# Kernel tuning notes

Measured on AMD Instinct MI355X. Metric: run time of the kernel, lower is better.

## Reference

```python
import jax, jax.numpy as jnp
import numpy as np

B, C, H, W = 128, 2048, 14, 14
K = 112          # num_concepts
NUM_CLASSES = 200


def setup_inputs() -> dict:
    key = jax.random.key(0)
    ks = jax.random.split(key, 8)
    x = jax.random.normal(ks[0], (B, C, H, W), dtype=jnp.float32)
    concepts = jax.random.normal(ks[1], (K, C), dtype=jnp.float32)
    modulation = jax.random.normal(ks[2], (1, C), dtype=jnp.float32)
    background = jax.random.normal(ks[3], (1, C), dtype=jnp.float32)
    # concept_fc: Linear(C, 1)
    w_cfc = jax.random.normal(ks[4], (1, C), dtype=jnp.float32) / np.sqrt(C)
    b_cfc = jnp.zeros((1,), dtype=jnp.float32)
    # label_fc: Linear(C*K, num_classes)
    w_lfc = jax.random.normal(ks[5], (NUM_CLASSES, C * K), dtype=jnp.float32) / np.sqrt(C * K)
    b_lfc = jnp.zeros((NUM_CLASSES,), dtype=jnp.float32)
    return {"x": x, "concepts": concepts, "modulation": modulation,
            "background": background, "w_cfc": w_cfc, "b_cfc": b_cfc,
            "w_lfc": w_lfc, "b_lfc": b_lfc}


def reference(x, concepts, modulation, background, w_cfc, b_cfc, w_lfc, b_lfc):
    b, c, h, w = x.shape
    n = h * w
    x_flat = x.reshape(b, c, n).transpose(0, 2, 1)          # [b, n, c]
    cpts_wbg = jnp.concatenate([concepts, background], 0)   # [k+1, c]

    # cdist p=2 via ||a||^2 + ||x||^2 - 2 a.x
    a_sq = jnp.sum(cpts_wbg * cpts_wbg, -1)                 # [k+1]
    x_sq = jnp.sum(x_flat * x_flat, -1)                     # [b, n]
    dots = jnp.einsum('kc,bnc->bkn', cpts_wbg, x_flat)      # [b, k+1, n]
    d2 = a_sq[None, :, None] + x_sq[:, None, :] - 2.0 * dots
    dists = jnp.sqrt(jnp.maximum(d2, 0.0))                  # [b, k+1, n]

    attn = jax.nn.softmax(-dists, axis=1)                   # softmax over concepts
    cpt_score_maps = attn.reshape(b, -1, h, w)              # [b, k+1, h, w]

    cpt_reprs = jnp.einsum('bkn,bnc->bkc', attn[:, :-1, :], x_flat)  # [b, k, c]
    cpt_logits = jax.nn.sigmoid(
        jnp.einsum('bkc,oc->bko', cpt_reprs, w_cfc) + b_cfc).squeeze(-1)  # [b, k]

    g = cpt_logits[..., None]                               # [b, k, 1]
    cpts_mixed = g * concepts[None] + (1.0 - g) * modulation[None]  # [b, k, c]
    label_logits = cpts_mixed.reshape(b, -1) @ w_lfc.T + b_lfc      # [b, classes]

    return cpt_score_maps, cpt_logits, label_logits
```

## Files before the change

### kernel.cpp

```cpp
#include <hip/hip_runtime.h>
#include <hip/hip_bf16.h>
#include <math.h>

#define B 128
#define C 2048
#define N 196
#define K 112
#define KB 113
#define MROWS 128
#define XWROW 113
#define NCLS 200
#define CKC (C * K)
#define MAIN_BLKS 128
#define PQ_BLKS 700
#define XSTEP 25088
#define IMGB (C * N * 4)

#define OUT1_OFF 2834944
#define OUT2_OFF 2849280

typedef __attribute__((ext_vector_type(8))) short bf16x8;
typedef __attribute__((ext_vector_type(4))) float f32x4;

__device__ inline unsigned cvtpk(float a, float b) {
    union { __hip_bfloat162 h; unsigned u; } c;
    c.h.x = __float2bfloat16(a);
    c.h.y = __float2bfloat16(b);
    return c.u;
}
__device__ inline const float* row_src(int row, const float* concepts,
                                       const float* background, const float* wcfc) {
    if (row < K) return concepts + (size_t)row * C;
    if (row == K) return background;
    if (row == XWROW) return wcfc;
    return nullptr;
}
__device__ __forceinline__ void gl16(const void* g, void* l) {
    __builtin_amdgcn_global_load_lds(
        (const __attribute__((address_space(1))) unsigned*)g,
        (__attribute__((address_space(3))) unsigned*)l, 16, 0, 0);
}
__device__ __forceinline__ void gl4(const void* g, void* l) {
    __builtin_amdgcn_global_load_lds(
        (const __attribute__((address_space(1))) unsigned*)g,
        (__attribute__((address_space(3))) unsigned*)l, 4, 0, 0);
}

__global__ __launch_bounds__(256)
void asq_kernel(const float* __restrict__ concepts, const float* __restrict__ background,
                const float* __restrict__ wcfc, float* __restrict__ asq) {
    const int row = blockIdx.x;
    const int tid = threadIdx.x;
    const float* src = row_src(row, concepts, background, wcfc);
    float local = 0.f;
    if (src) for (int i = tid; i < C; i += 256) { float v = src[i]; local += v * v; }
    for (int off = 32; off; off >>= 1) local += __shfl_down(local, off);
    __shared__ float red[4];
    if ((tid & 63) == 0) red[tid >> 6] = local;
    __syncthreads();
    if (tid == 0) asq[row] = red[0] + red[1] + red[2] + red[3];
}

__global__ __launch_bounds__(64)
void pack_kernel(const float* __restrict__ concepts, const float* __restrict__ background,
                 const float* __restrict__ wcfc, unsigned short* __restrict__ Afrag) {
    const int f = blockIdx.x;
    const int kwg = blockIdx.y;
    const int l = threadIdx.x;
    const int row = 16 * f + (l & 15);
    const int kb = 32 * kwg + 8 * (l >> 4);
    const float* src = row_src(row, concepts, background, wcfc);
    unsigned o[4] = {0u, 0u, 0u, 0u};
    if (src) {
        const float4 f0 = *reinterpret_cast<const float4*>(src + kb);
        const float4 f1 = *reinterpret_cast<const float4*>(src + kb + 4);
        o[0] = cvtpk(f0.x, f0.y); o[1] = cvtpk(f0.z, f0.w);
        o[2] = cvtpk(f1.x, f1.y); o[3] = cvtpk(f1.z, f1.w);
    }
    *reinterpret_cast<uint4*>(Afrag + (((size_t)kwg * 8 + f) * 64 + l) * 8) =
        make_uint4(o[0], o[1], o[2], o[3]);
}

__global__ __launch_bounds__(512)
void fused_kernel(const float* __restrict__ x,
                  const unsigned short* __restrict__ Afrag,
                  const float* __restrict__ asq_g,
                  float* __restrict__ out0,
                  float* __restrict__ lpart,
                  const float* __restrict__ wlfc,
                  const float* __restrict__ concepts,
                  const float* __restrict__ modulation,
                  float* __restrict__ Rm, float* __restrict__ Qs) {
    __shared__ __align__(16) char smem[61952];
    const int tid = threadIdx.x;
    const int lane = tid & 63;
    const int w = tid >> 6;
    const int blkid = blockIdx.x;

    if (blkid < MAIN_BLKS) {
        const int b = blkid;
        float* Xf = (float*)smem;
        char* Ab0 = smem + 25600;
        unsigned short* XT = (unsigned short*)(smem + 41984);
        float* xsqL = (float*)(smem + 58624);
        float* pmw = (float*)smem;
        float* xwL = (float*)(smem + 8192);

        const int lo = lane & 15, hi = lane >> 4;
        const char* xim = (const char*)x + (size_t)b * IMGB;
        const char* Ag = (const char*)Afrag;

        const bool act = tid < 416;
        const int h = (act && tid >= 208) ? 1 : 0;
        const int cc = act ? (tid - 208 * h) : 0;

        f32x4 acc[13];
#pragma unroll
        for (int ct = 0; ct < 13; ++ct) acc[ct] = (f32x4){0.f, 0.f, 0.f, 0.f};
        float xs = 0.f;

#define ISSUE_X(JJ) do {                                                        \
        const char* sx_ = xim + (size_t)(JJ) * XSTEP;                           \
        gl16(sx_ + (3 * w + 0) * 1024 + lane * 16, smem + (3 * w + 0) * 1024);  \
        gl16(sx_ + (3 * w + 1) * 1024 + lane * 16, smem + (3 * w + 1) * 1024);  \
        gl16(sx_ + (3 * w + 2) * 1024 + lane * 16, smem + (3 * w + 2) * 1024);  \
        if (w < 2) gl4(sx_ + 24576 + w * 256 + lane * 4,                        \
                       smem + 24576 + w * 256);                                 \
    } while (0)

#define ISSUE_A(JJ) do {                                                        \
        gl16(Ag + (size_t)(JJ) * 8192 + w * 1024 + lane * 16,                   \
             Ab0 + ((JJ) & 1) * 8192 + w * 1024);                               \
    } while (0)

#define VM0() do {                                                              \
        asm volatile("s_waitcnt vmcnt(0)" ::: "memory");                        \
        __builtin_amdgcn_sched_barrier(0);                                      \
    } while (0)

#define LBAR() do {                                                             \
        asm volatile("s_waitcnt lgkmcnt(0)" ::: "memory");                      \
        __builtin_amdgcn_s_barrier();                                           \
        __builtin_amdgcn_sched_barrier(0);                                      \
    } while (0)

#define CONVERT() do {                                                          \
        if (act) {                                                              \
            const float* xp_ = Xf + (16 * h) * 196 + cc;                        \
            float v_[16];                                                       \
            _Pragma("unroll")                                                   \
            for (int q_ = 0; q_ < 16; ++q_) v_[q_] = xp_[q_ * 196];             \
            _Pragma("unroll")                                                   \
            for (int q_ = 0; q_ < 16; ++q_) xs += v_[q_] * v_[q_];              \
            unsigned u_[8];                                                     \
            _Pragma("unroll")                                                   \
            for (int p_ = 0; p_ < 8; ++p_)                                      \
                u_[p_] = cvtpk(v_[2 * p_], v_[2 * p_ + 1]);                     \
            unsigned short* xt_ = XT + cc * 40 + h * 16;                        \
            *reinterpret_cast<uint4*>(xt_) = make_uint4(u_[0], u_[1], u_[2], u_[3]); \
            *reinterpret_cast<uint4*>(xt_ + 8) = make_uint4(u_[4], u_[5], u_[6], u_[7]); \
        }                                                                       \
    } while (0)

#define MFMA_STEP(JJ) do {                                                      \
        const char* Ab_ = Ab0 + ((JJ) & 1) * 8192;                              \
        const bf16x8 afr_ = *reinterpret_cast<const bf16x8*>(                   \
            Ab_ + ((w * 64 + lane) << 4));                                      \
        _Pragma("unroll")                                                       \
        for (int ct_ = 0; ct_ < 13; ++ct_) {                                    \
            const bf16x8 bfr_ = *reinterpret_cast<const bf16x8*>(               \
                (const char*)XT + (ct_ * 16 + lo) * 80 + hi * 16);              \
            acc[ct_] = __builtin_amdgcn_mfma_f32_16x16x32_bf16(                 \
                afr_, bfr_, acc[ct_], 0, 0, 0);                                 \
        }                                                                       \
    } while (0)

        ISSUE_X(0); ISSUE_A(0);
#pragma unroll 1
        for (int j = 0; j < 63; ++j) {
            VM0(); LBAR();
            CONVERT();
            LBAR();
            ISSUE_X(j + 1);
            MFMA_STEP(j);
            ISSUE_A(j + 1);
        }
        VM0(); LBAR(); CONVERT(); LBAR(); MFMA_STEP(63);

        __syncthreads();
        if (act) xsqL[h * 208 + cc] = xs;
        if (w == 7 && hi == 0) {
#pragma unroll
            for (int ct = 0; ct < 13; ++ct) xwL[ct * 16 + lo] = acc[ct][1];
        }
        __syncthreads();

        float xq[13];
#pragma unroll
        for (int ct = 0; ct < 13; ++ct) {
            const int c = ct * 16 + lo;
            xq[ct] = xsqL[c] + xsqL[208 + c];
        }
        float aq[4];
#pragma unroll
        for (int rr = 0; rr < 4; ++rr) aq[rr] = asq_g[16 * w + 4 * hi + rr];
        const bool v4 = (w < 7);

        float mct[13];
#pragma unroll
        for (int ct = 0; ct < 13; ++ct) {
#pragma unroll
            for (int rr = 0; rr < 4; ++rr) {
                const float d2 = aq[rr] + xq[ct] - 2.f * acc[ct][rr];
                acc[ct][rr] = -sqrtf(fmaxf(d2, 0.f));
            }
            float mv = -3.4e38f;
            if (v4) mv = fmaxf(fmaxf(acc[ct][0], acc[ct][1]),
                               fmaxf(acc[ct][2], acc[ct][3]));
            else if (hi == 0) mv = acc[ct][0];
            mv = fmaxf(mv, __shfl_xor(mv, 16));
            mv = fmaxf(mv, __shfl_xor(mv, 32));
            mct[ct] = mv;
        }
        if (hi == 0) {
#pragma unroll
            for (int ct = 0; ct < 13; ++ct) pmw[w * 208 + ct * 16 + lo] = mct[ct];
        }
        __syncthreads();
        float Mct[13];
#pragma unroll
        for (int ct = 0; ct < 13; ++ct) {
            float mm = -3.4e38f;
#pragma unroll
            for (int ww = 0; ww < 8; ++ww)
                mm = fmaxf(mm, pmw[ww * 208 + ct * 16 + lo]);
            Mct[ct] = mm;
        }
        __syncthreads();
        float sct[13];
#pragma unroll
        for (int ct = 0; ct < 13; ++ct) {
            float ss = 0.f;
#pragma unroll
            for (int rr = 0; rr < 4; ++rr) {
                const bool valid = v4 || (hi == 0 && rr == 0);
                const float e = valid ? __expf(acc[ct][rr] - Mct[ct]) : 0.f;
                acc[ct][rr] = e;
                ss += e;
            }
            ss += __shfl_xor(ss, 16);
            ss += __shfl_xor(ss, 32);
            sct[ct] = ss;
        }
        if (hi == 0) {
#pragma unroll
            for (int ct = 0; ct < 13; ++ct) pmw[w * 208 + ct * 16 + lo] = sct[ct];
        }
        __syncthreads();
        float inv[13];
#pragma unroll
        for (int ct = 0; ct < 13; ++ct) {
            float SS = 0.f;
#pragma unroll
            for (int ww = 0; ww < 8; ++ww) SS += pmw[ww * 208 + ct * 16 + lo];
            inv[ct] = 1.f / SS;
        }

        float* o0 = out0 + (size_t)b * KB * N;
#pragma unroll
        for (int ct = 0; ct < 13; ++ct) {
            const int c = ct * 16 + lo;
            const bool cv = c < N;
#pragma unroll
            for (int rr = 0; rr < 4; ++rr) {
                const int r = 16 * w + 4 * hi + rr;
                const bool valid = v4 || (hi == 0 && rr == 0);
                if (valid && cv) o0[(size_t)r * N + c] = acc[ct][rr] * inv[ct];
            }
        }
        if (v4) {
#pragma unroll
            for (int rr = 0; rr < 4; ++rr) {
                float pv = 0.f;
#pragma unroll
                for (int ct = 0; ct < 13; ++ct) {
                    const int c = ct * 16 + lo;
                    const float term = acc[ct][rr] * inv[ct] * xwL[c];
                    pv += (c < N) ? term : 0.f;
                }
                pv += __shfl_xor(pv, 1);
                pv += __shfl_xor(pv, 2);
                pv += __shfl_xor(pv, 4);
                pv += __shfl_xor(pv, 8);
                if (lo == 0) lpart[(size_t)b * K + 16 * w + 4 * hi + rr] = pv;
            }
        }
    } else {
        const int wb = (blkid - MAIN_BLKS) * 32 + w * 4;
#pragma unroll
        for (int q = 0; q < 4; ++q) {
            const int wid = wb + q;
            const int o = wid / K;
            const int k = wid % K;
            const float4* wp = reinterpret_cast<const float4*>(wlfc + (size_t)o * CKC + (size_t)k * C);
            const float4* cp = reinterpret_cast<const float4*>(concepts + (size_t)k * C);
            const float4* mp = reinterpret_cast<const float4*>(modulation);
            float s1 = 0.f, s2 = 0.f;
#pragma unroll
            for (int it = 0; it < 8; ++it) {
                const int idx = it * 64 + lane;
                const float4 w4 = wp[idx];
                const float4 c4 = cp[idx];
                const float4 m4 = mp[idx];
                s1 += w4.x * c4.x + w4.y * c4.y + w4.z * c4.z + w4.w * c4.w;
                s2 += w4.x * m4.x + w4.y * m4.y + w4.z * m4.z + w4.w * m4.w;
            }
            for (int off = 32; off; off >>= 1) {
                s1 += __shfl_down(s1, off);
                s2 += __shfl_down(s2, off);
            }
            if (lane == 0) { Rm[wid] = s1 - s2; Qs[wid] = s2; }
        }
    }
}

__global__ __launch_bounds__(256)
void final_kernel(const float* __restrict__ lpart, const float* __restrict__ bcfc,
                  const float* __restrict__ Rm, const float* __restrict__ Qs,
                  const float* __restrict__ blfc,
                  float* __restrict__ out1, float* __restrict__ out2) {
    const int b = blockIdx.x;
    const int tid = threadIdx.x;
    __shared__ float g_s[K];
    if (tid < K) {
        const float v = lpart[(size_t)b * K + tid] + bcfc[0];
        const float g = 1.f / (1.f + __expf(-v));
        out1[b * K + tid] = g;
        g_s[tid] = g;
    }
    __syncthreads();
    if (tid < NCLS) {
        float acc = blfc[tid];
        const float* rp = Rm + (size_t)tid * K;
        const float* qp = Qs + (size_t)tid * K;
        for (int k = 0; k < K; ++k) acc = fmaf(g_s[k], rp[k], acc) + qp[k];
        out2[b * NCLS + tid] = acc;
    }
}

extern "C" void kernel_launch(void* const* d_in, const int* in_sizes, int n_in,
                              void* d_out, int out_size, void* d_ws, size_t ws_size,
                              hipStream_t stream) {
    const float* x          = (const float*)d_in[0];
    const float* concepts   = (const float*)d_in[1];
    const float* modulation = (const float*)d_in[2];
    const float* background = (const float*)d_in[3];
    const float* wcfc       = (const float*)d_in[4];
    const float* bcfc       = (const float*)d_in[5];
    const float* wlfc       = (const float*)d_in[6];
    const float* blfc       = (const float*)d_in[7];

    float* out  = (float*)d_out;
    float* out0 = out;
    float* out1 = out + OUT1_OFF;
    float* out2 = out + OUT2_OFF;

    float* ws    = (float*)d_ws;
    float* asq   = ws;
    float* lpart = asq + MROWS;
    float* Rm    = lpart + (size_t)B * K;
    float* Qs    = Rm + NCLS * K;
    unsigned short* Afrag = (unsigned short*)(Qs + NCLS * K);

    asq_kernel<<<MROWS, 256, 0, stream>>>(concepts, background, wcfc, asq);
    pack_kernel<<<dim3(8, 64), 64, 0, stream>>>(concepts, background, wcfc, Afrag);
    fused_kernel<<<MAIN_BLKS + PQ_BLKS, 512, 0, stream>>>(
        x, Afrag, asq, out0, lpart, wlfc, concepts, modulation, Rm, Qs);
    final_kernel<<<B, 256, 0, stream>>>(lpart, bcfc, Rm, Qs, blfc, out1, out2);
}
```

Measured before the change: 121.3 us.

## Split channel reduction across four blocks per image with atomic accumulation

The main GEMM phase now splits the 2048-channel reduction into four chunks, so each image is handled by four blocks instead of one and grid parallelism grows from 128 to 512 main blocks. Partial dot products, x-squared sums and the background-weight products are accumulated with float atomics into the output buffer and workspace, which are zeroed by memsets beforehand. The distance, softmax and concept-logit epilogue moves to a separate softmax kernel that rereads the accumulated dots. This adds two memsets, one extra launch, many global atomics and an extra read-modify-write pass over the score map, and float atomics make the summation order nondeterministic.

```diff
diff --git a/kernel.cpp b/kernel.cpp
--- a/kernel.cpp
+++ b/kernel.cpp
@@ -11,7 +11,9 @@
 #define XWROW 113
 #define NCLS 200
 #define CKC (C * K)
-#define MAIN_BLKS 128
+#define NSPL 4
+#define ITERS 16
+#define MAIN_BLKS 512
 #define PQ_BLKS 700
 #define XSTEP 25088
 #define IMGB (C * N * 4)
@@ -84,35 +86,32 @@
 __global__ __launch_bounds__(512)
 void fused_kernel(const float* __restrict__ x,
                   const unsigned short* __restrict__ Afrag,
-                  const float* __restrict__ asq_g,
                   float* __restrict__ out0,
-                  float* __restrict__ lpart,
+                  float* __restrict__ xsq_ws, float* __restrict__ xw_ws,
                   const float* __restrict__ wlfc,
                   const float* __restrict__ concepts,
                   const float* __restrict__ modulation,
                   float* __restrict__ Rm, float* __restrict__ Qs) {
-    __shared__ __align__(16) char smem[61952];
+    __shared__ __align__(16) char smem[58624];
     const int tid = threadIdx.x;
     const int lane = tid & 63;
     const int w = tid >> 6;
     const int blkid = blockIdx.x;
 
     if (blkid < MAIN_BLKS) {
-        const int b = blkid;
+        const int b = blkid >> 2;
+        const int h = blkid & 3;
         float* Xf = (float*)smem;
         char* Ab0 = smem + 25600;
         unsigned short* XT = (unsigned short*)(smem + 41984);
-        float* xsqL = (float*)(smem + 58624);
-        float* pmw = (float*)smem;
-        float* xwL = (float*)(smem + 8192);
 
         const int lo = lane & 15, hi = lane >> 4;
         const char* xim = (const char*)x + (size_t)b * IMGB;
         const char* Ag = (const char*)Afrag;
 
         const bool act = tid < 416;
-        const int h = (act && tid >= 208) ? 1 : 0;
-        const int cc = act ? (tid - 208 * h) : 0;
+        const int h2 = (act && tid >= 208) ? 1 : 0;
+        const int cc = act ? (tid - 208 * h2) : 0;
 
         f32x4 acc[13];
 #pragma unroll
@@ -146,7 +145,7 @@
 
 #define CONVERT() do {                                                          \
         if (act) {                                                              \
-            const float* xp_ = Xf + (16 * h) * 196 + cc;                        \
+            const float* xp_ = Xf + (16 * h2) * 196 + cc;                       \
             float v_[16];                                                       \
             _Pragma("unroll")                                                   \
             for (int q_ = 0; q_ < 16; ++q_) v_[q_] = xp_[q_ * 196];             \
@@ -156,7 +155,7 @@
             _Pragma("unroll")                                                   \
             for (int p_ = 0; p_ < 8; ++p_)                                      \
                 u_[p_] = cvtpk(v_[2 * p_], v_[2 * p_ + 1]);                     \
-            unsigned short* xt_ = XT + cc * 40 + h * 16;                        \
+            unsigned short* xt_ = XT + cc * 40 + h2 * 16;                       \
             *reinterpret_cast<uint4*>(xt_) = make_uint4(u_[0], u_[1], u_[2], u_[3]); \
             *reinterpret_cast<uint4*>(xt_ + 8) = make_uint4(u_[4], u_[5], u_[6], u_[7]); \
         }                                                                       \
@@ -175,9 +174,11 @@
         }                                                                       \
     } while (0)
 
-        ISSUE_X(0); ISSUE_A(0);
+        const int j0 = h * ITERS;
+        ISSUE_X(j0); ISSUE_A(j0);
 #pragma unroll 1
-        for (int j = 0; j < 63; ++j) {
+        for (int jj = 0; jj < ITERS - 1; ++jj) {
+            const int j = j0 + jj;
             VM0(); LBAR();
             CONVERT();
             LBAR();
@@ -185,114 +186,23 @@
             MFMA_STEP(j);
             ISSUE_A(j + 1);
         }
-        VM0(); LBAR(); CONVERT(); LBAR(); MFMA_STEP(63);
-
-        __syncthreads();
-        if (act) xsqL[h * 208 + cc] = xs;
-        if (w == 7 && hi == 0) {
-#pragma unroll
-            for (int ct = 0; ct < 13; ++ct) xwL[ct * 16 + lo] = acc[ct][1];
-        }
-        __syncthreads();
-
-        float xq[13];
+        VM0(); LBAR(); CONVERT(); LBAR(); MFMA_STEP(j0 + ITERS - 1);
+
+        if (act) atomicAdd(&xsq_ws[(size_t)b * 208 + cc], xs);
+        const bool v4 = (w < 7);
+        float* od = out0 + (size_t)b * KB * N;
 #pragma unroll
         for (int ct = 0; ct < 13; ++ct) {
             const int c = ct * 16 + lo;
-            xq[ct] = xsqL[c] + xsqL[208 + c];
-        }
-        float aq[4];
-#pragma unroll
-        for (int rr = 0; rr < 4; ++rr) aq[rr] = asq_g[16 * w + 4 * hi + rr];
-        const bool v4 = (w < 7);
-
-        float mct[13];
-#pragma unroll
-        for (int ct = 0; ct < 13; ++ct) {
-#pragma unroll
-            for (int rr = 0; rr < 4; ++rr) {
-                const float d2 = aq[rr] + xq[ct] - 2.f * acc[ct][rr];
-                acc[ct][rr] = -sqrtf(fmaxf(d2, 0.f));
-            }
-            float mv = -3.4e38f;
-            if (v4) mv = fmaxf(fmaxf(acc[ct][0], acc[ct][1]),
-                               fmaxf(acc[ct][2], acc[ct][3]));
-            else if (hi == 0) mv = acc[ct][0];
-            mv = fmaxf(mv, __shfl_xor(mv, 16));
-            mv = fmaxf(mv, __shfl_xor(mv, 32));
-            mct[ct] = mv;
-        }
-        if (hi == 0) {
-#pragma unroll
-            for (int ct = 0; ct < 13; ++ct) pmw[w * 208 + ct * 16 + lo] = mct[ct];
-        }
-        __syncthreads();
-        float Mct[13];
-#pragma unroll
-        for (int ct = 0; ct < 13; ++ct) {
-            float mm = -3.4e38f;
-#pragma unroll
-            for (int ww = 0; ww < 8; ++ww)
-                mm = fmaxf(mm, pmw[ww * 208 + ct * 16 + lo]);
-            Mct[ct] = mm;
-        }
-        __syncthreads();
-        float sct[13];
-#pragma unroll
-        for (int ct = 0; ct < 13; ++ct) {
-            float ss = 0.f;
-#pragma unroll
-            for (int rr = 0; rr < 4; ++rr) {
-                const bool valid = v4 || (hi == 0 && rr == 0);
-                const float e = valid ? __expf(acc[ct][rr] - Mct[ct]) : 0.f;
-                acc[ct][rr] = e;
-                ss += e;
-            }
-            ss += __shfl_xor(ss, 16);
-            ss += __shfl_xor(ss, 32);
-            sct[ct] = ss;
-        }
-        if (hi == 0) {
-#pragma unroll
-            for (int ct = 0; ct < 13; ++ct) pmw[w * 208 + ct * 16 + lo] = sct[ct];
-        }
-        __syncthreads();
-        float inv[13];
-#pragma unroll
-        for (int ct = 0; ct < 13; ++ct) {
-            float SS = 0.f;
-#pragma unroll
-            for (int ww = 0; ww < 8; ++ww) SS += pmw[ww * 208 + ct * 16 + lo];
-            inv[ct] = 1.f / SS;
-        }
-
-        float* o0 = out0 + (size_t)b * KB * N;
-#pragma unroll
-        for (int ct = 0; ct < 13; ++ct) {
-            const int c = ct * 16 + lo;
-            const bool cv = c < N;
-#pragma unroll
-            for (int rr = 0; rr < 4; ++rr) {
-                const int r = 16 * w + 4 * hi + rr;
-                const bool valid = v4 || (hi == 0 && rr == 0);
-                if (valid && cv) o0[(size_t)r * N + c] = acc[ct][rr] * inv[ct];
-            }
-        }
-        if (v4) {
-#pragma unroll
-            for (int rr = 0; rr < 4; ++rr) {
-                float pv = 0.f;
-#pragma unroll
-                for (int ct = 0; ct < 13; ++ct) {
-                    const int c = ct * 16 + lo;
-                    const float term = acc[ct][rr] * inv[ct] * xwL[c];
-                    pv += (c < N) ? term : 0.f;
+            if (c < N) {
+#pragma unroll
+                for (int rr = 0; rr < 4; ++rr) {
+                    const int r = 16 * w + 4 * hi + rr;
+                    if (v4 || (hi == 0 && rr == 0))
+                        atomicAdd(&od[(size_t)r * N + c], acc[ct][rr]);
                 }
-                pv += __shfl_xor(pv, 1);
-                pv += __shfl_xor(pv, 2);
-                pv += __shfl_xor(pv, 4);
-                pv += __shfl_xor(pv, 8);
-                if (lo == 0) lpart[(size_t)b * K + 16 * w + 4 * hi + rr] = pv;
+                if (w == 7 && hi == 0)
+                    atomicAdd(&xw_ws[(size_t)b * 208 + c], acc[ct][1]);
             }
         }
     } else {
@@ -324,6 +234,137 @@
     }
 }
 
+__global__ __launch_bounds__(512)
+void softmax_kernel(float* __restrict__ out0,
+                    const float* __restrict__ xsq_ws, const float* __restrict__ xw_ws,
+                    const float* __restrict__ asq_g,
+                    float* __restrict__ lpart) {
+    __shared__ float pmw[8 * 208];
+    __shared__ float xsqL[208];
+    __shared__ float xwL[208];
+    const int b = blockIdx.x;
+    const int tid = threadIdx.x;
+    const int lane = tid & 63;
+    const int w = tid >> 6;
+    const int lo = lane & 15, hi = lane >> 4;
+
+    if (tid < 208) {
+        xsqL[tid] = xsq_ws[(size_t)b * 208 + tid];
+        xwL[tid] = xw_ws[(size_t)b * 208 + tid];
+    }
+    __syncthreads();
+
+    const bool v4 = (w < 7);
+    float* od = out0 + (size_t)b * KB * N;
+
+    f32x4 acc[13];
+    float aq[4];
+#pragma unroll
+    for (int rr = 0; rr < 4; ++rr) aq[rr] = asq_g[16 * w + 4 * hi + rr];
+
+#pragma unroll
+    for (int ct = 0; ct < 13; ++ct) {
+        const int c = ct * 16 + lo;
+        const bool cv = c < N;
+#pragma unroll
+        for (int rr = 0; rr < 4; ++rr) {
+            const int r = 16 * w + 4 * hi + rr;
+            const bool valid = v4 || (hi == 0 && rr == 0);
+            acc[ct][rr] = (valid && cv) ? od[(size_t)r * N + c] : 0.f;
+        }
+    }
+
+    float mct[13];
+#pragma unroll
+    for (int ct = 0; ct < 13; ++ct) {
+        const int c = ct * 16 + lo;
+#pragma unroll
+        for (int rr = 0; rr < 4; ++rr) {
+            const float d2 = aq[rr] + xsqL[c] - 2.f * acc[ct][rr];
+            acc[ct][rr] = -sqrtf(fmaxf(d2, 0.f));
+        }
+        float mv = -3.4e38f;
+        if (v4) mv = fmaxf(fmaxf(acc[ct][0], acc[ct][1]),
+                           fmaxf(acc[ct][2], acc[ct][3]));
+        else if (hi == 0) mv = acc[ct][0];
+        mv = fmaxf(mv, __shfl_xor(mv, 16));
+        mv = fmaxf(mv, __shfl_xor(mv, 32));
+        mct[ct] = mv;
+    }
+    if (hi == 0) {
+#pragma unroll
+        for (int ct = 0; ct < 13; ++ct) pmw[w * 208 + ct * 16 + lo] = mct[ct];
+    }
+    __syncthreads();
+    float Mct[13];
+#pragma unroll
+    for (int ct = 0; ct < 13; ++ct) {
+        float mm = -3.4e38f;
+#pragma unroll
+        for (int ww = 0; ww < 8; ++ww)
+            mm = fmaxf(mm, pmw[ww * 208 + ct * 16 + lo]);
+        Mct[ct] = mm;
+    }
+    __syncthreads();
+    float sct[13];
+#pragma unroll
+    for (int ct = 0; ct < 13; ++ct) {
+        float ss = 0.f;
+#pragma unroll
+        for (int rr = 0; rr < 4; ++rr) {
+            const bool valid = v4 || (hi == 0 && rr == 0);
+            const float e = valid ? __expf(acc[ct][rr] - Mct[ct]) : 0.f;
+            acc[ct][rr] = e;
+            ss += e;
+        }
+        ss += __shfl_xor(ss, 16);
+        ss += __shfl_xor(ss, 32);
+        sct[ct] = ss;
+    }
+    if (hi == 0) {
+#pragma unroll
+        for (int ct = 0; ct < 13; ++ct) pmw[w * 208 + ct * 16 + lo] = sct[ct];
+    }
+    __syncthreads();
+    float inv[13];
+#pragma unroll
+    for (int ct = 0; ct < 13; ++ct) {
+        float SS = 0.f;
+#pragma unroll
+        for (int ww = 0; ww < 8; ++ww) SS += pmw[ww * 208 + ct * 16 + lo];
+        inv[ct] = 1.f / SS;
+    }
+
+#pragma unroll
+    for (int ct = 0; ct < 13; ++ct) {
+        const int c = ct * 16 + lo;
+        const bool cv = c < N;
+#pragma unroll
+        for (int rr = 0; rr < 4; ++rr) {
+            const int r = 16 * w + 4 * hi + rr;
+            const bool valid = v4 || (hi == 0 && rr == 0);
+            if (valid && cv) od[(size_t)r * N + c] = acc[ct][rr] * inv[ct];
+        }
+    }
+    if (v4) {
+#pragma unroll
+        for (int rr = 0; rr < 4; ++rr) {
+            float pv = 0.f;
+#pragma unroll
+            for (int ct = 0; ct < 13; ++ct) {
+                const int c = ct * 16 + lo;
+                const float term = acc[ct][rr] * inv[ct] * xwL[c];
+                pv += (c < N) ? term : 0.f;
+            }
+            pv += __shfl_xor(pv, 1);
+            pv += __shfl_xor(pv, 2);
+            pv += __shfl_xor(pv, 4);
+            pv += __shfl_xor(pv, 8);
+            if (lo == 0) lpart[(size_t)b * K + 16 * w + 4 * hi + rr] = pv;
+        }
+    }
+}
+
 __global__ __launch_bounds__(256)
 void final_kernel(const float* __restrict__ lpart, const float* __restrict__ bcfc,
                   const float* __restrict__ Rm, const float* __restrict__ Qs,
@@ -365,16 +406,22 @@
     float* out1 = out + OUT1_OFF;
     float* out2 = out + OUT2_OFF;
 
-    float* ws    = (float*)d_ws;
-    float* asq   = ws;
-    float* lpart = asq + MROWS;
-    float* Rm    = lpart + (size_t)B * K;
-    float* Qs    = Rm + NCLS * K;
-    unsigned short* Afrag = (unsigned short*)(Qs + NCLS * K);
+    float* ws     = (float*)d_ws;
+    float* asq    = ws;
+    float* lpart  = asq + MROWS;
+    float* Rm     = lpart + (size_t)B * K;
+    float* Qs     = Rm + NCLS * K;
+    float* xsq_ws = Qs + NCLS * K;
+    float* xw_ws  = xsq_ws + (size_t)B * 208;
+    unsigned short* Afrag = (unsigned short*)(xw_ws + (size_t)B * 208);
+
+    hipMemsetAsync(out0, 0, (size_t)OUT1_OFF * sizeof(float), stream);
+    hipMemsetAsync(xsq_ws, 0, (size_t)2 * B * 208 * sizeof(float), stream);
 
     asq_kernel<<<MROWS, 256, 0, stream>>>(concepts, background, wcfc, asq);
     pack_kernel<<<dim3(8, 64), 64, 0, stream>>>(concepts, background, wcfc, Afrag);
     fused_kernel<<<MAIN_BLKS + PQ_BLKS, 512, 0, stream>>>(
-        x, Afrag, asq, out0, lpart, wlfc, concepts, modulation, Rm, Qs);
+        x, Afrag, out0, xsq_ws, xw_ws, wlfc, concepts, modulation, Rm, Qs);
+    softmax_kernel<<<B, 512, 0, stream>>>(out0, xsq_ws, xw_ws, asq, lpart);
     final_kernel<<<B, 256, 0, stream>>>(lpart, bcfc, Rm, Qs, blfc, out1, out2);
 }
```

Result: slower. 199.5 us (+64.5%).

## Deepen load pipeline and retile MFMA work as 2x2 row/column wave grid

Applied to the files above, without the earlier changes.

The main loop now triple-buffers the fp32 x tiles and quad-buffers the A fragments, issuing loads two steps ahead. It also double-buffers the transposed bf16 tile so the conversion of step j overlaps the MFMA of step j-1, with one barrier per iteration instead of two. Waves are regrouped into a 4x2 grid where each wave computes two row tiles by up to seven column tiles, reusing B fragments across two A fragments. Shared memory grows to about 140KB, which limits occupancy, and the softmax reductions are reworked for the new tiling with a final cross-wave sum for lpart.

```diff
diff --git a/kernel.cpp b/kernel.cpp
--- a/kernel.cpp
+++ b/kernel.cpp
@@ -15,6 +15,10 @@
 #define PQ_BLKS 700
 #define XSTEP 25088
 #define IMGB (C * N * 4)
+#define XFSLOT 25600
+#define ABASE 76800
+#define XTBASE 109568
+#define SMEMSZ 142848
 
 #define OUT1_OFF 2834944
 #define OUT2_OFF 2849280
@@ -39,11 +43,6 @@
     __builtin_amdgcn_global_load_lds(
         (const __attribute__((address_space(1))) unsigned*)g,
         (__attribute__((address_space(3))) unsigned*)l, 16, 0, 0);
-}
-__device__ __forceinline__ void gl4(const void* g, void* l) {
-    __builtin_amdgcn_global_load_lds(
-        (const __attribute__((address_space(1))) unsigned*)g,
-        (__attribute__((address_space(3))) unsigned*)l, 4, 0, 0);
 }
 
 __global__ __launch_bounds__(256)
@@ -91,7 +90,7 @@
                   const float* __restrict__ concepts,
                   const float* __restrict__ modulation,
                   float* __restrict__ Rm, float* __restrict__ Qs) {
-    __shared__ __align__(16) char smem[61952];
+    __shared__ __align__(16) char smem[SMEMSZ];
     const int tid = threadIdx.x;
     const int lane = tid & 63;
     const int w = tid >> 6;
@@ -99,54 +98,40 @@
 
     if (blkid < MAIN_BLKS) {
         const int b = blkid;
-        float* Xf = (float*)smem;
-        char* Ab0 = smem + 25600;
-        unsigned short* XT = (unsigned short*)(smem + 41984);
-        float* xsqL = (float*)(smem + 58624);
-        float* pmw = (float*)smem;
-        float* xwL = (float*)(smem + 8192);
-
         const int lo = lane & 15, hi = lane >> 4;
+        const int wr = w & 3, wc = w >> 2;
+        const int nct = 7 - wc;
+
         const char* xim = (const char*)x + (size_t)b * IMGB;
         const char* Ag = (const char*)Afrag;
+        unsigned short* XTb = (unsigned short*)(smem + XTBASE);
 
         const bool act = tid < 416;
-        const int h = (act && tid >= 208) ? 1 : 0;
-        const int cc = act ? (tid - 208 * h) : 0;
-
-        f32x4 acc[13];
-#pragma unroll
-        for (int ct = 0; ct < 13; ++ct) acc[ct] = (f32x4){0.f, 0.f, 0.f, 0.f};
+        const int h2 = (act && tid >= 208) ? 1 : 0;
+        const int cc = act ? (tid - 208 * h2) : 0;
+
+        f32x4 acc[2][7];
+#pragma unroll
+        for (int rt = 0; rt < 2; ++rt)
+#pragma unroll
+            for (int ct = 0; ct < 7; ++ct) acc[rt][ct] = (f32x4){0.f, 0.f, 0.f, 0.f};
         float xs = 0.f;
 
-#define ISSUE_X(JJ) do {                                                        \
+#define ISSUE(JJ) do {                                                          \
         const char* sx_ = xim + (size_t)(JJ) * XSTEP;                           \
-        gl16(sx_ + (3 * w + 0) * 1024 + lane * 16, smem + (3 * w + 0) * 1024);  \
-        gl16(sx_ + (3 * w + 1) * 1024 + lane * 16, smem + (3 * w + 1) * 1024);  \
-        gl16(sx_ + (3 * w + 2) * 1024 + lane * 16, smem + (3 * w + 2) * 1024);  \
-        if (w < 2) gl4(sx_ + 24576 + w * 256 + lane * 4,                        \
-                       smem + 24576 + w * 256);                                 \
+        char* xb_ = smem + ((JJ) % 3) * XFSLOT;                                 \
+        gl16(sx_ + (3 * w + 0) * 1024 + lane * 16, xb_ + (3 * w + 0) * 1024);   \
+        gl16(sx_ + (3 * w + 1) * 1024 + lane * 16, xb_ + (3 * w + 1) * 1024);   \
+        gl16(sx_ + (3 * w + 2) * 1024 + lane * 16, xb_ + (3 * w + 2) * 1024);   \
+        if (w == 0) gl16(sx_ + 24064 + lane * 16, xb_ + 24064);                 \
+        gl16(Ag + (size_t)(JJ) * 8192 + w * 1024 + lane * 16,                   \
+             smem + ABASE + ((JJ) % 4) * 8192 + w * 1024);                      \
     } while (0)
 
-#define ISSUE_A(JJ) do {                                                        \
-        gl16(Ag + (size_t)(JJ) * 8192 + w * 1024 + lane * 16,                   \
-             Ab0 + ((JJ) & 1) * 8192 + w * 1024);                               \
-    } while (0)
-
-#define VM0() do {                                                              \
-        asm volatile("s_waitcnt vmcnt(0)" ::: "memory");                        \
-        __builtin_amdgcn_sched_barrier(0);                                      \
-    } while (0)
-
-#define LBAR() do {                                                             \
-        asm volatile("s_waitcnt lgkmcnt(0)" ::: "memory");                      \
-        __builtin_amdgcn_s_barrier();                                           \
-        __builtin_amdgcn_sched_barrier(0);                                      \
-    } while (0)
-
-#define CONVERT() do {                                                          \
+#define CONVERT(JJ) do {                                                        \
         if (act) {                                                              \
-            const float* xp_ = Xf + (16 * h) * 196 + cc;                        \
+            const float* xp_ = (const float*)(smem + ((JJ) % 3) * XFSLOT)       \
+                               + (16 * h2) * 196 + cc;                          \
             float v_[16];                                                       \
             _Pragma("unroll")                                                   \
             for (int q_ = 0; q_ < 16; ++q_) v_[q_] = xp_[q_ * 196];             \
@@ -156,145 +141,183 @@
             _Pragma("unroll")                                                   \
             for (int p_ = 0; p_ < 8; ++p_)                                      \
                 u_[p_] = cvtpk(v_[2 * p_], v_[2 * p_ + 1]);                     \
-            unsigned short* xt_ = XT + cc * 40 + h * 16;                        \
+            unsigned short* xt_ = XTb + ((JJ) & 1) * 8320 + cc * 40 + h2 * 16;  \
             *reinterpret_cast<uint4*>(xt_) = make_uint4(u_[0], u_[1], u_[2], u_[3]); \
             *reinterpret_cast<uint4*>(xt_ + 8) = make_uint4(u_[4], u_[5], u_[6], u_[7]); \
         }                                                                       \
     } while (0)
 
 #define MFMA_STEP(JJ) do {                                                      \
-        const char* Ab_ = Ab0 + ((JJ) & 1) * 8192;                              \
-        const bf16x8 afr_ = *reinterpret_cast<const bf16x8*>(                   \
-            Ab_ + ((w * 64 + lane) << 4));                                      \
+        const char* Ab_ = smem + ABASE + ((JJ) % 4) * 8192;                     \
+        bf16x8 af0_ = *reinterpret_cast<const bf16x8*>(                         \
+            Ab_ + ((2 * wr + 0) * 64 + lane) * 16);                             \
+        bf16x8 af1_ = *reinterpret_cast<const bf16x8*>(                         \
+            Ab_ + ((2 * wr + 1) * 64 + lane) * 16);                             \
+        const char* xt_ = (const char*)XTb + ((JJ) & 1) * 16640;                \
         _Pragma("unroll")                                                       \
-        for (int ct_ = 0; ct_ < 13; ++ct_) {                                    \
-            const bf16x8 bfr_ = *reinterpret_cast<const bf16x8*>(               \
-                (const char*)XT + (ct_ * 16 + lo) * 80 + hi * 16);              \
-            acc[ct_] = __builtin_amdgcn_mfma_f32_16x16x32_bf16(                 \
-                afr_, bfr_, acc[ct_], 0, 0, 0);                                 \
+        for (int ct_ = 0; ct_ < 7; ++ct_) {                                     \
+            if (ct_ < nct) {                                                    \
+                const bf16x8 bf_ = *reinterpret_cast<const bf16x8*>(            \
+                    xt_ + ((wc * 7 + ct_) * 16 + lo) * 80 + hi * 16);           \
+                acc[0][ct_] = __builtin_amdgcn_mfma_f32_16x16x32_bf16(          \
+                    af0_, bf_, acc[0][ct_], 0, 0, 0);                           \
+                acc[1][ct_] = __builtin_amdgcn_mfma_f32_16x16x32_bf16(          \
+                    af1_, bf_, acc[1][ct_], 0, 0, 0);                           \
+            }                                                                   \
         }                                                                       \
     } while (0)
 
-        ISSUE_X(0); ISSUE_A(0);
+        ISSUE(0); ISSUE(1);
 #pragma unroll 1
-        for (int j = 0; j < 63; ++j) {
-            VM0(); LBAR();
-            CONVERT();
-            LBAR();
-            ISSUE_X(j + 1);
-            MFMA_STEP(j);
-            ISSUE_A(j + 1);
-        }
-        VM0(); LBAR(); CONVERT(); LBAR(); MFMA_STEP(63);
-
-        __syncthreads();
-        if (act) xsqL[h * 208 + cc] = xs;
-        if (w == 7 && hi == 0) {
-#pragma unroll
-            for (int ct = 0; ct < 13; ++ct) xwL[ct * 16 + lo] = acc[ct][1];
-        }
-        __syncthreads();
-
-        float xq[13];
-#pragma unroll
-        for (int ct = 0; ct < 13; ++ct) {
-            const int c = ct * 16 + lo;
-            xq[ct] = xsqL[c] + xsqL[208 + c];
-        }
-        float aq[4];
-#pragma unroll
-        for (int rr = 0; rr < 4; ++rr) aq[rr] = asq_g[16 * w + 4 * hi + rr];
-        const bool v4 = (w < 7);
-
-        float mct[13];
-#pragma unroll
-        for (int ct = 0; ct < 13; ++ct) {
-#pragma unroll
-            for (int rr = 0; rr < 4; ++rr) {
-                const float d2 = aq[rr] + xq[ct] - 2.f * acc[ct][rr];
-                acc[ct][rr] = -sqrtf(fmaxf(d2, 0.f));
-            }
-            float mv = -3.4e38f;
-            if (v4) mv = fmaxf(fmaxf(acc[ct][0], acc[ct][1]),
-                               fmaxf(acc[ct][2], acc[ct][3]));
-            else if (hi == 0) mv = acc[ct][0];
-            mv = fmaxf(mv, __shfl_xor(mv, 16));
-            mv = fmaxf(mv, __shfl_xor(mv, 32));
-            mct[ct] = mv;
+        for (int j = 0; j < 64; ++j) {
+            asm volatile("s_waitcnt lgkmcnt(0)" ::: "memory");
+            if (j < 63) {
+                if (w == 0) asm volatile("s_waitcnt vmcnt(5)" ::: "memory");
+                else        asm volatile("s_waitcnt vmcnt(4)" ::: "memory");
+            } else {
+                asm volatile("s_waitcnt vmcnt(0)" ::: "memory");
+            }
+            __builtin_amdgcn_s_barrier();
+            __builtin_amdgcn_sched_barrier(0);
+            if (j < 62) ISSUE(j + 2);
+            CONVERT(j);
+            if (j > 0) MFMA_STEP(j - 1);
+        }
+        asm volatile("s_waitcnt lgkmcnt(0)" ::: "memory");
+        __builtin_amdgcn_s_barrier();
+        __builtin_amdgcn_sched_barrier(0);
+        MFMA_STEP(63);
+
+        float* pmw  = (float*)smem;
+        float* xsqL = (float*)(smem + 3584);
+        float* xwL  = (float*)(smem + 5376);
+        float* lpw  = (float*)(smem + 6272);
+
+        __syncthreads();
+        if (act) xsqL[h2 * 208 + cc] = xs;
+        if (wr == 3 && hi == 0) {
+#pragma unroll
+            for (int ct = 0; ct < 7; ++ct)
+                if (ct < nct) xwL[112 * wc + 16 * ct + lo] = acc[1][ct][1];
+        }
+        __syncthreads();
+
+        float xq[7];
+#pragma unroll
+        for (int ct = 0; ct < 7; ++ct)
+            if (ct < nct) {
+                const int c = 112 * wc + 16 * ct + lo;
+                xq[ct] = xsqL[c] + xsqL[208 + c];
+            }
+        float aq0[4], aq1[4];
+#pragma unroll
+        for (int rr = 0; rr < 4; ++rr) {
+            aq0[rr] = asq_g[32 * wr + 4 * hi + rr];
+            aq1[rr] = asq_g[32 * wr + 16 + 4 * hi + rr];
+        }
+
+        float mct[7];
+#pragma unroll
+        for (int ct = 0; ct < 7; ++ct) {
+            if (ct < nct) {
+                float mv = -3.4e38f;
+#pragma unroll
+                for (int rr = 0; rr < 4; ++rr) {
+                    const float L0 = -sqrtf(fmaxf(aq0[rr] + xq[ct] - 2.f * acc[0][ct][rr], 0.f));
+                    const float L1 = -sqrtf(fmaxf(aq1[rr] + xq[ct] - 2.f * acc[1][ct][rr], 0.f));
+                    acc[0][ct][rr] = L0;
+                    acc[1][ct][rr] = L1;
+                    mv = fmaxf(mv, L0);
+                    const bool valid1 = (wr < 3) || (hi == 0 && rr == 0);
+                    if (valid1) mv = fmaxf(mv, L1);
+                }
+                mv = fmaxf(mv, __shfl_xor(mv, 16));
+                mv = fmaxf(mv, __shfl_xor(mv, 32));
+                mct[ct] = mv;
+            }
         }
         if (hi == 0) {
 #pragma unroll
-            for (int ct = 0; ct < 13; ++ct) pmw[w * 208 + ct * 16 + lo] = mct[ct];
-        }
-        __syncthreads();
-        float Mct[13];
-#pragma unroll
-        for (int ct = 0; ct < 13; ++ct) {
-            float mm = -3.4e38f;
-#pragma unroll
-            for (int ww = 0; ww < 8; ++ww)
-                mm = fmaxf(mm, pmw[ww * 208 + ct * 16 + lo]);
-            Mct[ct] = mm;
-        }
-        __syncthreads();
-        float sct[13];
-#pragma unroll
-        for (int ct = 0; ct < 13; ++ct) {
-            float ss = 0.f;
-#pragma unroll
-            for (int rr = 0; rr < 4; ++rr) {
-                const bool valid = v4 || (hi == 0 && rr == 0);
-                const float e = valid ? __expf(acc[ct][rr] - Mct[ct]) : 0.f;
-                acc[ct][rr] = e;
-                ss += e;
-            }
-            ss += __shfl_xor(ss, 16);
-            ss += __shfl_xor(ss, 32);
-            sct[ct] = ss;
-        }
-        if (hi == 0) {
-#pragma unroll
-            for (int ct = 0; ct < 13; ++ct) pmw[w * 208 + ct * 16 + lo] = sct[ct];
-        }
-        __syncthreads();
-        float inv[13];
-#pragma unroll
-        for (int ct = 0; ct < 13; ++ct) {
-            float SS = 0.f;
-#pragma unroll
-            for (int ww = 0; ww < 8; ++ww) SS += pmw[ww * 208 + ct * 16 + lo];
-            inv[ct] = 1.f / SS;
-        }
-
-        float* o0 = out0 + (size_t)b * KB * N;
-#pragma unroll
-        for (int ct = 0; ct < 13; ++ct) {
-            const int c = ct * 16 + lo;
-            const bool cv = c < N;
-#pragma unroll
-            for (int rr = 0; rr < 4; ++rr) {
-                const int r = 16 * w + 4 * hi + rr;
-                const bool valid = v4 || (hi == 0 && rr == 0);
-                if (valid && cv) o0[(size_t)r * N + c] = acc[ct][rr] * inv[ct];
-            }
-        }
-        if (v4) {
-#pragma unroll
-            for (int rr = 0; rr < 4; ++rr) {
-                float pv = 0.f;
-#pragma unroll
-                for (int ct = 0; ct < 13; ++ct) {
-                    const int c = ct * 16 + lo;
-                    const float term = acc[ct][rr] * inv[ct] * xwL[c];
-                    pv += (c < N) ? term : 0.f;
+            for (int ct = 0; ct < 7; ++ct)
+                if (ct < nct) pmw[wr * 208 + 112 * wc + 16 * ct + lo] = mct[ct];
+        }
+        __syncthreads();
+        float Mct[7];
+#pragma unroll
+        for (int ct = 0; ct < 7; ++ct)
+            if (ct < nct) {
+                const int c = 112 * wc + 16 * ct + lo;
+                Mct[ct] = fmaxf(fmaxf(pmw[c], pmw[208 + c]),
+                                fmaxf(pmw[416 + c], pmw[624 + c]));
+            }
+        __syncthreads();
+#pragma unroll
+        for (int ct = 0; ct < 7; ++ct) {
+            if (ct < nct) {
+                float ss = 0.f;
+#pragma unroll
+                for (int rr = 0; rr < 4; ++rr) {
+                    const float e0 = __expf(acc[0][ct][rr] - Mct[ct]);
+                    acc[0][ct][rr] = e0;
+                    ss += e0;
+                    const bool valid1 = (wr < 3) || (hi == 0 && rr == 0);
+                    const float e1 = valid1 ? __expf(acc[1][ct][rr] - Mct[ct]) : 0.f;
+                    acc[1][ct][rr] = e1;
+                    ss += e1;
                 }
-                pv += __shfl_xor(pv, 1);
-                pv += __shfl_xor(pv, 2);
-                pv += __shfl_xor(pv, 4);
-                pv += __shfl_xor(pv, 8);
-                if (lo == 0) lpart[(size_t)b * K + 16 * w + 4 * hi + rr] = pv;
-            }
-        }
+                ss += __shfl_xor(ss, 16);
+                ss += __shfl_xor(ss, 32);
+                if (hi == 0) pmw[wr * 208 + 112 * wc + 16 * ct + lo] = ss;
+            }
+        }
+        __syncthreads();
+        float inv[7];
+#pragma unroll
+        for (int ct = 0; ct < 7; ++ct)
+            if (ct < nct) {
+                const int c = 112 * wc + 16 * ct + lo;
+                inv[ct] = 1.f / (pmw[c] + pmw[208 + c] + pmw[416 + c] + pmw[624 + c]);
+            }
+
+        float* od = out0 + (size_t)b * KB * N;
+#pragma unroll
+        for (int ct = 0; ct < 7; ++ct) {
+            if (ct < nct) {
+                const int c = 112 * wc + 16 * ct + lo;
+                const bool cv = c < N;
+#pragma unroll
+                for (int rr = 0; rr < 4; ++rr) {
+                    const int r0 = 32 * wr + 4 * hi + rr;
+                    if (cv) od[(size_t)r0 * N + c] = acc[0][ct][rr] * inv[ct];
+                    const bool valid1 = (wr < 3) || (hi == 0 && rr == 0);
+                    if (valid1 && cv) od[(size_t)(r0 + 16) * N + c] = acc[1][ct][rr] * inv[ct];
+                }
+            }
+        }
+#pragma unroll
+        for (int rr = 0; rr < 4; ++rr) {
+            float pv0 = 0.f, pv1 = 0.f;
+#pragma unroll
+            for (int ct = 0; ct < 7; ++ct) {
+                if (ct < nct) {
+                    const int c = 112 * wc + 16 * ct + lo;
+                    const float t0 = acc[0][ct][rr] * inv[ct] * xwL[c];
+                    const float t1 = acc[1][ct][rr] * inv[ct] * xwL[c];
+                    pv0 += (c < N) ? t0 : 0.f;
+                    pv1 += (c < N) ? t1 : 0.f;
+                }
+            }
+            pv0 += __shfl_xor(pv0, 1); pv0 += __shfl_xor(pv0, 2);
+            pv0 += __shfl_xor(pv0, 4); pv0 += __shfl_xor(pv0, 8);
+            pv1 += __shfl_xor(pv1, 1); pv1 += __shfl_xor(pv1, 2);
+            pv1 += __shfl_xor(pv1, 4); pv1 += __shfl_xor(pv1, 8);
+            if (lo == 0) {
+                lpw[wc * 128 + 32 * wr + 4 * hi + rr] = pv0;
+                if (wr < 3) lpw[wc * 128 + 32 * wr + 16 + 4 * hi + rr] = pv1;
+            }
+        }
+        __syncthreads();
+        if (tid < K) lpart[(size_t)b * K + tid] = lpw[tid] + lpw[128 + tid];
     } else {
         const int wb = (blkid - MAIN_BLKS) * 32 + w * 4;
 #pragma unroll
```

After: 128.9 us. 6.3% more time.

## Process two channel chunks per main-loop iteration to halve barrier count

Applied to the files above, without the earlier changes.

The main GEMM loop now stages two 32-channel x chunks and two A fragment tiles per iteration, converting both and running two MFMA steps between barrier pairs. This halves the number of vmcnt waits and workgroup barriers across the 64 chunks. The tail 4-byte loads are replaced by a single 16-byte load that covers the remainder. LDS use grows to about 117 KB per block, which limits blocks per CU, and adds more register pressure.

```diff
diff --git a/kernel.cpp b/kernel.cpp
--- a/kernel.cpp
+++ b/kernel.cpp
@@ -15,6 +15,10 @@
 #define PQ_BLKS 700
 #define XSTEP 25088
 #define IMGB (C * N * 4)
+#define XFSLOT 25600
+#define ABASE 51200
+#define XTBASE 83968
+#define SMEMSZ 117248
 
 #define OUT1_OFF 2834944
 #define OUT2_OFF 2849280
@@ -39,11 +43,6 @@
     __builtin_amdgcn_global_load_lds(
         (const __attribute__((address_space(1))) unsigned*)g,
         (__attribute__((address_space(3))) unsigned*)l, 16, 0, 0);
-}
-__device__ __forceinline__ void gl4(const void* g, void* l) {
-    __builtin_amdgcn_global_load_lds(
-        (const __attribute__((address_space(1))) unsigned*)g,
-        (__attribute__((address_space(3))) unsigned*)l, 4, 0, 0);
 }
 
 __global__ __launch_bounds__(256)
@@ -91,7 +90,7 @@
                   const float* __restrict__ concepts,
                   const float* __restrict__ modulation,
                   float* __restrict__ Rm, float* __restrict__ Qs) {
-    __shared__ __align__(16) char smem[61952];
+    __shared__ __align__(16) char smem[SMEMSZ];
     const int tid = threadIdx.x;
     const int lane = tid & 63;
     const int w = tid >> 6;
@@ -99,38 +98,38 @@
 
     if (blkid < MAIN_BLKS) {
         const int b = blkid;
-        float* Xf = (float*)smem;
-        char* Ab0 = smem + 25600;
-        unsigned short* XT = (unsigned short*)(smem + 41984);
-        float* xsqL = (float*)(smem + 58624);
-        float* pmw = (float*)smem;
-        float* xwL = (float*)(smem + 8192);
+        unsigned short* XTu = (unsigned short*)(smem + XTBASE);
 
         const int lo = lane & 15, hi = lane >> 4;
         const char* xim = (const char*)x + (size_t)b * IMGB;
         const char* Ag = (const char*)Afrag;
 
         const bool act = tid < 416;
-        const int h = (act && tid >= 208) ? 1 : 0;
-        const int cc = act ? (tid - 208 * h) : 0;
+        const int h2 = (act && tid >= 208) ? 1 : 0;
+        const int cc = act ? (tid - 208 * h2) : 0;
 
         f32x4 acc[13];
 #pragma unroll
         for (int ct = 0; ct < 13; ++ct) acc[ct] = (f32x4){0.f, 0.f, 0.f, 0.f};
         float xs = 0.f;
 
-#define ISSUE_X(JJ) do {                                                        \
-        const char* sx_ = xim + (size_t)(JJ) * XSTEP;                           \
-        gl16(sx_ + (3 * w + 0) * 1024 + lane * 16, smem + (3 * w + 0) * 1024);  \
-        gl16(sx_ + (3 * w + 1) * 1024 + lane * 16, smem + (3 * w + 1) * 1024);  \
-        gl16(sx_ + (3 * w + 2) * 1024 + lane * 16, smem + (3 * w + 2) * 1024);  \
-        if (w < 2) gl4(sx_ + 24576 + w * 256 + lane * 4,                        \
-                       smem + 24576 + w * 256);                                 \
-    } while (0)
-
-#define ISSUE_A(JJ) do {                                                        \
-        gl16(Ag + (size_t)(JJ) * 8192 + w * 1024 + lane * 16,                   \
-             Ab0 + ((JJ) & 1) * 8192 + w * 1024);                               \
+#define ISSUE_X2(JJ) do {                                                       \
+        _Pragma("unroll")                                                       \
+        for (int s_ = 0; s_ < 2; ++s_) {                                        \
+            const char* sx_ = xim + (size_t)(2 * (JJ) + s_) * XSTEP;            \
+            char* xb_ = smem + s_ * XFSLOT;                                     \
+            gl16(sx_ + (3 * w + 0) * 1024 + lane * 16, xb_ + (3 * w + 0) * 1024);\
+            gl16(sx_ + (3 * w + 1) * 1024 + lane * 16, xb_ + (3 * w + 1) * 1024);\
+            gl16(sx_ + (3 * w + 2) * 1024 + lane * 16, xb_ + (3 * w + 2) * 1024);\
+            if (w == 0) gl16(sx_ + 24064 + lane * 16, xb_ + 24064);             \
+        }                                                                       \
+    } while (0)
+
+#define ISSUE_A2(JJ) do {                                                       \
+        _Pragma("unroll")                                                       \
+        for (int s_ = 0; s_ < 2; ++s_)                                          \
+            gl16(Ag + (size_t)(2 * (JJ) + s_) * 8192 + w * 1024 + lane * 16,    \
+                 smem + ABASE + ((JJ) & 1) * 16384 + s_ * 8192 + w * 1024);     \
     } while (0)
 
 #define VM0() do {                                                              \
@@ -144,9 +143,10 @@
         __builtin_amdgcn_sched_barrier(0);                                      \
     } while (0)
 
-#define CONVERT() do {                                                          \
+#define CONVERT(S) do {                                                         \
         if (act) {                                                              \
-            const float* xp_ = Xf + (16 * h) * 196 + cc;                        \
+            const float* xp_ = (const float*)(smem + (S) * XFSLOT)              \
+                               + (16 * h2) * 196 + cc;                          \
             float v_[16];                                                       \
             _Pragma("unroll")                                                   \
             for (int q_ = 0; q_ < 16; ++q_) v_[q_] = xp_[q_ * 196];             \
@@ -156,39 +156,44 @@
             _Pragma("unroll")                                                   \
             for (int p_ = 0; p_ < 8; ++p_)                                      \
                 u_[p_] = cvtpk(v_[2 * p_], v_[2 * p_ + 1]);                     \
-            unsigned short* xt_ = XT + cc * 40 + h * 16;                        \
+            unsigned short* xt_ = XTu + (S) * 8320 + cc * 40 + h2 * 16;         \
             *reinterpret_cast<uint4*>(xt_) = make_uint4(u_[0], u_[1], u_[2], u_[3]); \
             *reinterpret_cast<uint4*>(xt_ + 8) = make_uint4(u_[4], u_[5], u_[6], u_[7]); \
         }                                                                       \
     } while (0)
 
-#define MFMA_STEP(JJ) do {                                                      \
-        const char* Ab_ = Ab0 + ((JJ) & 1) * 8192;                              \
+#define MFMA_STEP(S, JJ) do {                                                   \
+        const char* Ab_ = smem + ABASE + ((JJ) & 1) * 16384 + (S) * 8192;       \
         const bf16x8 afr_ = *reinterpret_cast<const bf16x8*>(                   \
             Ab_ + ((w * 64 + lane) << 4));                                      \
+        const char* xt_ = (const char*)XTu + (S) * 16640;                       \
         _Pragma("unroll")                                                       \
         for (int ct_ = 0; ct_ < 13; ++ct_) {                                    \
             const bf16x8 bfr_ = *reinterpret_cast<const bf16x8*>(               \
-                (const char*)XT + (ct_ * 16 + lo) * 80 + hi * 16);              \
+                xt_ + (ct_ * 16 + lo) * 80 + hi * 16);                          \
             acc[ct_] = __builtin_amdgcn_mfma_f32_16x16x32_bf16(                 \
                 afr_, bfr_, acc[ct_], 0, 0, 0);                                 \
         }                                                                       \
     } while (0)
 
-        ISSUE_X(0); ISSUE_A(0);
+        ISSUE_X2(0); ISSUE_A2(0);
 #pragma unroll 1
-        for (int j = 0; j < 63; ++j) {
+        for (int jj = 0; jj < 32; ++jj) {
             VM0(); LBAR();
-            CONVERT();
+            CONVERT(0); CONVERT(1);
             LBAR();
-            ISSUE_X(j + 1);
-            MFMA_STEP(j);
-            ISSUE_A(j + 1);
-        }
-        VM0(); LBAR(); CONVERT(); LBAR(); MFMA_STEP(63);
-
-        __syncthreads();
-        if (act) xsqL[h * 208 + cc] = xs;
+            if (jj < 31) ISSUE_X2(jj + 1);
+            MFMA_STEP(0, jj);
+            if (jj < 31) ISSUE_A2(jj + 1);
+            MFMA_STEP(1, jj);
+        }
+
+        float* pmw  = (float*)smem;
+        float* xsqL = (float*)(smem + 6656);
+        float* xwL  = (float*)(smem + 8320);
+
+        __syncthreads();
+        if (act) xsqL[h2 * 208 + cc] = xs;
         if (w == 7 && hi == 0) {
 #pragma unroll
             for (int ct = 0; ct < 13; ++ct) xwL[ct * 16 + lo] = acc[ct][1];
```

After: 115.4 us. 1.05x faster.
